# Optimization experiments

Measured on AMD Instinct MI355X. Metric: run time of the kernel, lower is better.

## Reference

```python
import jax, jax.numpy as jnp
import numpy as np
from jax import lax

# model dims (must match init_kwargs)
NB, E, G0, G1 = 1, 64, 32, 256          # num_blocks, embed_dim, grid rows, grid cols
DM, DIN, DS, DC, DTR = 2048, 4096, 16, 4, 128  # d_model, d_inner, d_state, d_conv, dt_rank
PS, ST, KD = (2, 16), (2, 16), (31, 31)
B, C, T = 8, 64, 4096


def setup_inputs() -> dict:
    key = jax.random.key(0)
    ks = jax.random.split(key, 4)
    rng = np.random.default_rng(0)

    def w(*s, fan=None):
        fan = fan if fan is not None else s[-1]
        return jnp.asarray((rng.standard_normal(s) / np.sqrt(fan)).astype(np.float32))

    # mamba_ssm-style dt bias init: softplus(bias) ~ Uniform-log in [1e-3, 0.1]
    dt = np.exp(rng.uniform(size=(NB, 2, DIN)) * (np.log(0.1) - np.log(1e-3)) + np.log(1e-3))
    dt = np.clip(dt, 1e-4, None)
    bdt = jnp.asarray((dt + np.log(-np.expm1(-dt))).astype(np.float32))
    A_log = jnp.asarray(np.broadcast_to(np.log(np.arange(1, DS + 1, dtype=np.float32)), (NB, 2, DIN, DS)).copy())

    return {
        'x': jax.random.normal(ks[0], (B, C, T), dtype=jnp.float32),
        'mask': jax.random.uniform(ks[1], (B, C, T)) < 0.5,
        'proj_w': w(E, 1, PS[0], PS[1], fan=PS[0] * PS[1]),
        'proj_b': jnp.zeros((E,), jnp.float32),
        'pos_embed': 0.02 * jax.random.normal(ks[2], (1, G1, DM), dtype=jnp.float32),
        'in_proj_w': w(NB, 2, 2 * DIN, DM, fan=DM),
        'conv_w': w(NB, 2, DIN, DC, fan=DC),
        'conv_b': jnp.zeros((NB, 2, DIN), jnp.float32),
        'x_proj_w': w(NB, 2, DTR + 2 * DS, DIN, fan=DIN),
        'dt_proj_w': w(NB, 2, DIN, DTR, fan=DTR),
        'dt_proj_b': bdt,
        'A_log': A_log,
        'Dp': jnp.ones((NB, 2, DIN), jnp.float32),
        'out_proj_w': w(NB, 2, DM, DIN, fan=DIN),
        'ln_g': jnp.ones((NB, DM), jnp.float32),
        'ln_b': jnp.zeros((NB, DM), jnp.float32),
        'dec_conv_w': w(1, 1, KD[0], KD[1], fan=KD[0] * KD[1]),
        'convT_w': w(E, 1, PS[0], PS[1], fan=E),
        'convT_b': jnp.zeros((1,), jnp.float32),
    }


def _layernorm(x, g, b, eps=1e-5):
    m = jnp.mean(x, -1, keepdims=True)
    v = jnp.var(x, -1, keepdims=True)
    return (x - m) * lax.rsqrt(v + eps) * g + b


def _mamba(h, Win, Wc, bc, Wx, Wdt, bdt, Alog, Dp, Wout):
    # h: [B, L, DM]; faithful port of mamba_ssm Mamba (selective scan reference path)
    xz = jnp.einsum('bld,ed->ble', h, Win)               # [B, L, 2*DIN]
    xc, z = jnp.split(xz, 2, axis=-1)
    xc = xc.swapaxes(1, 2)                               # [B, DIN, L]
    xc = lax.conv_general_dilated(xc, Wc[:, None, :], (1,), ((DC - 1, 0),),
                                  dimension_numbers=('NCH', 'OIH', 'NCH'),
                                  feature_group_count=DIN) + bc[None, :, None]
    u = jax.nn.silu(xc).swapaxes(1, 2)                   # [B, L, DIN]
    x_dbl = jnp.einsum('bld,ed->ble', u, Wx)             # [B, L, DTR+2*DS]
    dt = jax.nn.softplus(jnp.einsum('blr,dr->bld', x_dbl[..., :DTR], Wdt) + bdt)
    Bm = x_dbl[..., DTR:DTR + DS]                        # [B, L, DS]
    Cm = x_dbl[..., DTR + DS:]                           # [B, L, DS]
    A = -jnp.exp(Alog)                                   # [DIN, DS]

    def step(hst, inp):
        dt_t, B_t, C_t, u_t = inp                        # [B,DIN],[B,DS],[B,DS],[B,DIN]
        dA = jnp.exp(dt_t[..., None] * A)                # [B, DIN, DS]
        hst = hst * dA + (dt_t * u_t)[..., None] * B_t[:, None, :]
        return hst, jnp.einsum('bds,bs->bd', hst, C_t)

    h0 = jnp.zeros((h.shape[0], DIN, DS), h.dtype)
    xs = (dt.swapaxes(0, 1), Bm.swapaxes(0, 1), Cm.swapaxes(0, 1), u.swapaxes(0, 1))
    _, ys = lax.scan(step, h0, xs)
    y = ys.swapaxes(0, 1) + u * Dp                       # [B, L, DIN]
    y = y * jax.nn.silu(z)
    return jnp.einsum('bld,ed->ble', y, Wout)            # [B, L, DM]


def _forward(x, mask, proj_w, proj_b, pos_embed, in_proj_w, conv_w, conv_b,
             x_proj_w, dt_proj_w, dt_proj_b, A_log, Dp, out_proj_w,
             ln_g, ln_b, dec_conv_w, convT_w, convT_b):
    xm = jnp.where(mask, 0.0, x)                         # x_masked[mask] = 0
    p = lax.conv_general_dilated(xm[:, None], proj_w, ST, 'VALID',
                                 dimension_numbers=('NCHW', 'OIHW', 'NCHW'))
    p = p + proj_b[None, :, None, None]                  # [B, E, G0, G1]
    h = p.reshape(p.shape[0], E * G0, G1).transpose(0, 2, 1) + pos_embed  # [B, G1, DM]
    for i in range(NB):
        a_f = (in_proj_w[i, 0], conv_w[i, 0], conv_b[i, 0], x_proj_w[i, 0], dt_proj_w[i, 0],
               dt_proj_b[i, 0], A_log[i, 0], Dp[i, 0], out_proj_w[i, 0])
        a_r = (in_proj_w[i, 1], conv_w[i, 1], conv_b[i, 1], x_proj_w[i, 1], dt_proj_w[i, 1],
               dt_proj_b[i, 1], A_log[i, 1], Dp[i, 1], out_proj_w[i, 1])
        o = _mamba(h, *a_f) + jnp.flip(_mamba(jnp.flip(h, 1), *a_r), 1)  # bidirectional add
        h = _layernorm(h + o, ln_g[i], ln_b[i])
    # Decoder
    d = lax.conv_general_dilated(h[:, None], dec_conv_w, (1, 1),
                                 (((KD[0] - 1) // 2,) * 2, ((KD[1] - 1) // 2,) * 2),
                                 dimension_numbers=('NCHW', 'OIHW', 'NCHW'))
    d = d[:, 0].transpose(0, 2, 1).reshape(-1, E, G0, G1)
    # ConvTranspose2d(E->1, k=PS, stride=ST) as lhs-dilated conv with flipped kernel
    wct = jnp.flip(convT_w, (2, 3)).swapaxes(0, 1)       # [1, E, kh, kw]
    rec = lax.conv_general_dilated(d, wct, (1, 1),
                                   ((PS[0] - 1, PS[0] - 1), (PS[1] - 1, PS[1] - 1)),
                                   lhs_dilation=ST,
                                   dimension_numbers=('NCHW', 'OIHW', 'NCHW'))
    rec = rec + convT_b[None, :, None, None]
    return rec[:, 0], x                                  # (x_reconstructed, x_original)


def reference(x, mask, proj_w, proj_b, pos_embed, in_proj_w, conv_w, conv_b,
              x_proj_w, dt_proj_w, dt_proj_b, A_log, Dp, out_proj_w,
              ln_g, ln_b, dec_conv_w, convT_w, convT_b):
    return _forward(x, mask, proj_w, proj_b, pos_embed, in_proj_w, conv_w, conv_b,
                    x_proj_w, dt_proj_w, dt_proj_b, A_log, Dp, out_proj_w,
                    ln_g, ln_b, dec_conv_w, convT_w, convT_b)
```

## Files before the change

kernel.cpp:

```cpp
#include <hip/hip_runtime.h>
#include <hip/hip_bf16.h>
#include <math.h>

typedef unsigned short u16;
typedef __attribute__((ext_vector_type(8))) short bf16x8;
typedef __attribute__((ext_vector_type(4))) float f32x4;

__device__ __forceinline__ float b2f(u16 v) {
  unsigned u = ((unsigned)v) << 16;
  return __builtin_bit_cast(float, u);
}
__device__ __forceinline__ u16 f2b(float f) {
  unsigned u = __builtin_bit_cast(unsigned, f);
  unsigned r = u + 0x7fffu + ((u >> 16) & 1u);
  return (u16)(r >> 16);
}
__device__ __forceinline__ void gload_lds16(const u16* g, u16* l) {
  __builtin_amdgcn_global_load_lds(
      (const __attribute__((address_space(1))) void*)g,
      (__attribute__((address_space(3))) void*)l, 16, 0, 0);
}

__global__ __launch_bounds__(256) void cvt_bf16_k(const float* __restrict__ s,
                                                  u16* __restrict__ d, int n4) {
  int i = blockIdx.x * 256 + threadIdx.x;
  if (i < n4) {
    float4 v = ((const float4*)s)[i];
    ushort4 o;
    o.x = f2b(v.x); o.y = f2b(v.y); o.z = f2b(v.z); o.w = f2b(v.w);
    ((ushort4*)d)[i] = o;
  }
}

__global__ __launch_bounds__(256) void toeplitz_k(
    const float* __restrict__ kw, u16* __restrict__ tb)
{
  int i = blockIdx.x * 256 + threadIdx.x;
  if (i >= 31744) return;
  int k = i & 31, n = (i >> 5) & 15, h = (i >> 9) & 1, ki = i >> 10;
  int t = h * 32 + k - n;
  float v = (t >= 0 && t <= 30) ? kw[ki * 31 + t] : 0.f;
  tb[i] = f2b(v);
}

__global__ __launch_bounds__(256) void patchify_k(
    const float* __restrict__ x, const int* __restrict__ mask,
    const float* __restrict__ pw, const float* __restrict__ pb,
    const float* __restrict__ pos, float* __restrict__ h, u16* __restrict__ hb)
{
  int g1 = blockIdx.x, b = blockIdx.y, tid = threadIdx.x;
  __shared__ float sX[64 * 17];
  __shared__ float sW[2048];
  for (int i = tid; i < 64 * 16; i += 256) {
    int r = i >> 4, c = i & 15;
    int gi = (b * 64 + r) * 4096 + g1 * 16 + c;
    sX[r * 17 + c] = mask[gi] ? 0.f : x[gi];
  }
  for (int i = tid; i < 2048; i += 256) sW[i] = pw[i];
  __syncthreads();
  for (int m = tid; m < 2048; m += 256) {
    int e = m >> 5, g0 = m & 31;
    float acc = pb[e];
    const float* w = &sW[e * 32];
#pragma unroll
    for (int kh = 0; kh < 2; ++kh)
#pragma unroll
      for (int kw = 0; kw < 16; ++kw)
        acc += sX[(2 * g0 + kh) * 17 + kw] * w[kh * 16 + kw];
    float v = acc + pos[g1 * 2048 + m];
    long o = ((long)b * 256 + g1) * 2048 + m;
    h[o] = v;
    hb[o] = f2b(v);
  }
}

__global__ __launch_bounds__(512, 2) void gemm256_k(
    const u16* __restrict__ A0,
    const u16* __restrict__ B0, long bStride,
    u16* __restrict__ C0, long cStride,
    const float* __restrict__ cw,
    const float* __restrict__ cb,
    u16* __restrict__ ub)
{
  constexpr int K = 2048, N = 8192, LDA = 2048;
  __shared__ __align__(16) u16 lds[67584];
  u16* As = lds;
  u16* Bs = lds + 32768;
  const int dir = blockIdx.z;
  const u16* A = A0;
  const u16* B = B0 + (long)dir * bStride;
  u16* C = C0 + (long)dir * cStride;
  const int flip = dir;

  const int tid = threadIdx.x;
  const int wave = tid >> 6, lane = tid & 63;
  const int wr = wave >> 2, wc = wave & 3;
  const int bm = blockIdx.y * 256, bn = blockIdx.x * 256;
  const int lr = lane & 15, lq = lane >> 4;

  f32x4 acc[8][4];
#pragma unroll
  for (int i = 0; i < 8; ++i)
#pragma unroll
    for (int j = 0; j < 4; ++j) acc[i][j] = (f32x4){0.f, 0.f, 0.f, 0.f};

  auto stage = [&](int buf, int kt) {
    int k0 = kt << 6;
#pragma unroll
    for (int hf = 0; hf < 2; ++hf)
#pragma unroll
      for (int j = 0; j < 2; ++j) {
        int g = j * 512 + tid;
        int rl = hf * 128 + (g >> 3);
        int gr = (g & 7) ^ ((g >> 3) & 7);
        int ar = flip ? (bm + 255 - rl) : (bm + rl);
        gload_lds16(A + (long)ar * LDA + k0 + gr * 8,
                    &As[buf * 16384 + hf * 8192 + g * 8]);
        gload_lds16(B + (long)(bn + rl) * K + k0 + gr * 8,
                    &Bs[buf * 16384 + hf * 8192 + g * 8]);
      }
  };

  const int nk = K >> 6;
  stage(0, 0);
  for (int kt = 0; kt < nk; ++kt) {
    __builtin_amdgcn_s_barrier();
    __builtin_amdgcn_sched_barrier(0);
    if (kt + 1 < nk) {
      stage((kt + 1) & 1, kt + 1);
      asm volatile("s_waitcnt vmcnt(16)" ::: "memory");
    } else {
      asm volatile("s_waitcnt vmcnt(0)" ::: "memory");
    }
    __builtin_amdgcn_sched_barrier(0);
    __builtin_amdgcn_s_barrier();
    __builtin_amdgcn_sched_barrier(0);
    const int buf = kt & 1;
#pragma unroll
    for (int h = 0; h < 2; ++h) {
      bf16x8 av[8], bv[4];
#pragma unroll
      for (int i = 0; i < 8; ++i) {
        int row = wr * 128 + i * 16 + lr;
        av[i] = *(const bf16x8*)
            &As[buf * 16384 + ((row * 64 + h * 32 + lq * 8) ^ ((row & 7) << 3))];
      }
#pragma unroll
      for (int j = 0; j < 4; ++j) {
        int row = wc * 64 + j * 16 + lr;
        bv[j] = *(const bf16x8*)
            &Bs[buf * 16384 + ((row * 64 + h * 32 + lq * 8) ^ ((row & 7) << 3))];
      }
      __builtin_amdgcn_s_setprio(1);
#pragma unroll
      for (int i = 0; i < 8; ++i)
#pragma unroll
        for (int j = 0; j < 4; ++j)
          acc[i][j] = __builtin_amdgcn_mfma_f32_16x16x32_bf16(
              av[i], bv[j], acc[i][j], 0, 0, 0);
      __builtin_amdgcn_s_setprio(0);
    }
  }

  if (bn < 4096) {
    __syncthreads();
    u16* tile = lds;
#pragma unroll
    for (int i = 0; i < 8; ++i) {
      int r0 = wr * 128 + i * 16 + lq * 4;
#pragma unroll
      for (int j = 0; j < 4; ++j) {
        int col = wc * 64 + j * 16 + lr;
        f32x4 v = acc[i][j];
#pragma unroll
        for (int r = 0; r < 4; ++r)
          tile[(r0 + r) * 264 + col] = f2b(v[r]);
      }
    }
    __syncthreads();
    const int rgrp = tid >> 5, c8 = tid & 31;
    const int d0 = bn + c8 * 8;
    float wv0[8], wv1[8], wv2[8], wv3[8], cbv[8];
#pragma unroll
    for (int e = 0; e < 8; ++e) {
      const float4 wq = *(const float4*)(cw + ((long)dir * 4096 + d0 + e) * 4);
      wv0[e] = wq.x; wv1[e] = wq.y; wv2[e] = wq.z; wv3[e] = wq.w;
      cbv[e] = cb[dir * 4096 + d0 + e];
    }
    const int l0 = rgrp * 16;
    float w0[8], w1[8], w2[8];
#pragma unroll
    for (int e = 0; e < 8; ++e) { w0[e] = 0.f; w1[e] = 0.f; w2[e] = 0.f; }
    if (rgrp > 0) {
      bf16x8 t0 = *(const bf16x8*)&tile[(l0 - 3) * 264 + c8 * 8];
      bf16x8 t1 = *(const bf16x8*)&tile[(l0 - 2) * 264 + c8 * 8];
      bf16x8 t2 = *(const bf16x8*)&tile[(l0 - 1) * 264 + c8 * 8];
#pragma unroll
      for (int e = 0; e < 8; ++e) {
        w0[e] = b2f((u16)t0[e]); w1[e] = b2f((u16)t1[e]); w2[e] = b2f((u16)t2[e]);
      }
    }
    long ubase = ((long)(dir * 8 + blockIdx.y) * 256 + l0) * 4096 + d0;
#pragma unroll
    for (int l = 0; l < 16; ++l) {
      bf16x8 t = *(const bf16x8*)&tile[(l0 + l) * 264 + c8 * 8];
      float cur[8];
#pragma unroll
      for (int e = 0; e < 8; ++e) cur[e] = b2f((u16)t[e]);
      bf16x8 ov;
#pragma unroll
      for (int e = 0; e < 8; ++e) {
        float a = cbv[e] + wv0[e] * w0[e] + wv1[e] * w1[e] + wv2[e] * w2[e] +
                  wv3[e] * cur[e];
        ov[e] = (short)f2b(a / (1.f + __expf(-a)));
      }
      *(bf16x8*)(ub + ubase + (long)l * 4096) = ov;
#pragma unroll
      for (int e = 0; e < 8; ++e) { w0[e] = w1[e]; w1[e] = w2[e]; w2[e] = cur[e]; }
    }
  } else {
#pragma unroll
    for (int i = 0; i < 8; ++i) {
      int r0 = bm + wr * 128 + i * 16 + lq * 4;
#pragma unroll
      for (int j = 0; j < 4; ++j) {
        int col = bn + wc * 64 + j * 16 + lr;
        f32x4 v = acc[i][j];
#pragma unroll
        for (int r = 0; r < 4; ++r)
          C[(long)(r0 + r) * N + col] = f2b(v[r]);
      }
    }
  }
}

__global__ __launch_bounds__(512, 2) void gemm256o_k(
    const u16* __restrict__ Y0,
    const u16* __restrict__ W0,
    u16* __restrict__ part)
{
  constexpr int LDK = 4096;
  __shared__ __align__(16) u16 lds[65536];
  u16* As = lds;
  u16* Bs = lds + 32768;
  const int dir = blockIdx.z >> 1, split = blockIdx.z & 1;
  const u16* A = Y0 + (long)dir * 2048 * 4096;
  const u16* B = W0 + (long)dir * 2048 * 4096;
  u16* C = part + (long)blockIdx.z * 4194304;
  const int kbase = split << 11;

  const int tid = threadIdx.x;
  const int wave = tid >> 6, lane = tid & 63;
  const int wr = wave >> 2, wc = wave & 3;
  const int bm = blockIdx.y * 256, bn = blockIdx.x * 256;
  const int lr = lane & 15, lq = lane >> 4;

  f32x4 acc[8][4];
#pragma unroll
  for (int i = 0; i < 8; ++i)
#pragma unroll
    for (int j = 0; j < 4; ++j) acc[i][j] = (f32x4){0.f, 0.f, 0.f, 0.f};

  auto stage = [&](int buf, int kt) {
    int k0 = kbase + (kt << 6);
#pragma unroll
    for (int hf = 0; hf < 2; ++hf)
#pragma unroll
      for (int j = 0; j < 2; ++j) {
        int g = j * 512 + tid;
        int rl = hf * 128 + (g >> 3);
        int gr = (g & 7) ^ ((g >> 3) & 7);
        gload_lds16(A + (long)(bm + rl) * LDK + k0 + gr * 8,
                    &As[buf * 16384 + hf * 8192 + g * 8]);
        gload_lds16(B + (long)(bn + rl) * LDK + k0 + gr * 8,
                    &Bs[buf * 16384 + hf * 8192 + g * 8]);
      }
  };

  const int nk = 32;
  stage(0, 0);
  for (int kt = 0; kt < nk; ++kt) {
    __builtin_amdgcn_s_barrier();
    __builtin_amdgcn_sched_barrier(0);
    if (kt + 1 < nk) {
      stage((kt + 1) & 1, kt + 1);
      asm volatile("s_waitcnt vmcnt(16)" ::: "memory");
    } else {
      asm volatile("s_waitcnt vmcnt(0)" ::: "memory");
    }
    __builtin_amdgcn_sched_barrier(0);
    __builtin_amdgcn_s_barrier();
    __builtin_amdgcn_sched_barrier(0);
    const int buf = kt & 1;
#pragma unroll
    for (int h = 0; h < 2; ++h) {
      bf16x8 av[8], bv[4];
#pragma unroll
      for (int i = 0; i < 8; ++i) {
        int row = wr * 128 + i * 16 + lr;
        av[i] = *(const bf16x8*)
            &As[buf * 16384 + ((row * 64 + h * 32 + lq * 8) ^ ((row & 7) << 3))];
      }
#pragma unroll
      for (int j = 0; j < 4; ++j) {
        int row = wc * 64 + j * 16 + lr;
        bv[j] = *(const bf16x8*)
            &Bs[buf * 16384 + ((row * 64 + h * 32 + lq * 8) ^ ((row & 7) << 3))];
      }
      __builtin_amdgcn_s_setprio(1);
#pragma unroll
      for (int i = 0; i < 8; ++i)
#pragma unroll
        for (int j = 0; j < 4; ++j)
          acc[i][j] = __builtin_amdgcn_mfma_f32_16x16x32_bf16(
              av[i], bv[j], acc[i][j], 0, 0, 0);
      __builtin_amdgcn_s_setprio(0);
    }
  }

#pragma unroll
  for (int i = 0; i < 8; ++i) {
    int r0 = bm + wr * 128 + i * 16 + lq * 4;
#pragma unroll
    for (int j = 0; j < 4; ++j) {
      int col = bn + wc * 64 + j * 16 + lr;
      f32x4 v = acc[i][j];
#pragma unroll
      for (int r = 0; r < 4; ++r)
        C[(long)(r0 + r) * 2048 + col] = f2b(v[r]);
    }
  }
}

template <int EPI, int F32OUT, int BFOUT>
__global__ __launch_bounds__(256) void mfma_gemm_k(
    const u16* __restrict__ A0, long aStride,
    const u16* __restrict__ B0, long bStride,
    float* __restrict__ C0, long cStride,
    u16* __restrict__ Cb0, long cbStride,
    const float* __restrict__ bias0, int biasStride,
    int N, int K, int lda, int flipDir1)
{
  __shared__ __align__(16) u16 As[2][4096];
  __shared__ __align__(16) u16 Bs[2][4096];
  const int dir = blockIdx.z;
  const u16* A = A0 + (long)dir * aStride;
  const u16* B = B0 + (long)dir * bStride;
  float* C = F32OUT ? (C0 + (long)dir * cStride) : nullptr;
  u16* Cb = BFOUT ? (Cb0 + (long)dir * cbStride) : nullptr;
  const float* bias = (EPI == 1) ? (bias0 + (long)dir * biasStride) : nullptr;
  const int flip = flipDir1 && (dir == 1);

  const int tid = threadIdx.x;
  const int wave = tid >> 6, lane = tid & 63;
  const int wr = wave >> 1, wc = wave & 1;
  const int bm = blockIdx.y * 128, bn = blockIdx.x * 128;
  const int lr = lane & 15, lq = lane >> 4;

  f32x4 acc[4][4];
#pragma unroll
  for (int i = 0; i < 4; ++i)
#pragma unroll
    for (int j = 0; j < 4; ++j) acc[i][j] = (f32x4){0.f, 0.f, 0.f, 0.f};

  const int nk = K >> 5;

  auto stage = [&](int buf, int k0) {
#pragma unroll
    for (int iss = 0; iss < 2; ++iss) {
      int ob = wave * 2048 + iss * 1024 + lane * 16;
      int row = ob >> 6, kb = (ob >> 4) & 3;
      int rg = bm + row;
      rg = flip ? ((rg & ~255) | (255 - (rg & 255))) : rg;
      gload_lds16(A + (long)rg * lda + k0 + kb * 8,
                  &As[buf][wave * 1024 + iss * 512]);
      int rb = bn + row; rb = (rb < N) ? rb : (N - 1);
      gload_lds16(B + (long)rb * K + k0 + kb * 8,
                  &Bs[buf][wave * 1024 + iss * 512]);
    }
  };

  stage(0, 0);
  for (int kt = 0; kt < nk; ++kt) {
    __syncthreads();
    if (kt + 1 < nk) stage((kt + 1) & 1, (kt + 1) << 5);
    const int buf = kt & 1;
    bf16x8 av[4], bv[4];
#pragma unroll
    for (int i = 0; i < 4; ++i)
      av[i] = *(const bf16x8*)&As[buf][(wr * 64 + i * 16 + lr) * 32 + lq * 8];
#pragma unroll
    for (int j = 0; j < 4; ++j)
      bv[j] = *(const bf16x8*)&Bs[buf][(wc * 64 + j * 16 + lr) * 32 + lq * 8];
#pragma unroll
    for (int i = 0; i < 4; ++i)
#pragma unroll
      for (int j = 0; j < 4; ++j)
        acc[i][j] = __builtin_amdgcn_mfma_f32_16x16x32_bf16(av[i], bv[j],
                                                            acc[i][j], 0, 0, 0);
  }

#pragma unroll
  for (int i = 0; i < 4; ++i) {
    int r0 = bm + wr * 64 + i * 16 + lq * 4;
#pragma unroll
    for (int j = 0; j < 4; ++j) {
      int col = bn + wc * 64 + j * 16 + lr;
      if (col < N) {
        f32x4 v = acc[i][j];
#pragma unroll
        for (int r = 0; r < 4; ++r) {
          float xv = v[r];
          if (EPI == 1) {
            xv += bias[col];
            xv = (xv > 20.f) ? xv : log1pf(expf(xv));
          }
          if (F32OUT) C[(long)(r0 + r) * N + col] = xv;
          if (BFOUT) Cb[(long)(r0 + r) * N + col] = f2b(xv);
        }
      }
    }
  }
}

__global__ __launch_bounds__(256) void xdbl_part_k(
    const u16* __restrict__ ubf, const u16* __restrict__ Wxbf,
    float* __restrict__ part)
{
  __shared__ __align__(16) u16 As[2][4096];
  __shared__ __align__(16) u16 Bs[2][4096];
  const int dir = blockIdx.z >> 2, split = blockIdx.z & 3;
  const u16* A = ubf + (long)dir * 2048 * 4096;
  const u16* B = Wxbf + (long)dir * 160 * 4096;
  float* C = part + (long)blockIdx.z * 327680;
  const int tid = threadIdx.x;
  const int wave = tid >> 6, lane = tid & 63;
  const int wr = wave >> 1, wc = wave & 1;
  const int bm = blockIdx.y * 128, bn = blockIdx.x * 128;
  const int lr = lane & 15, lq = lane >> 4;

  f32x4 acc[4][4];
#pragma unroll
  for (int i = 0; i < 4; ++i)
#pragma unroll
    for (int j = 0; j < 4; ++j) acc[i][j] = (f32x4){0.f, 0.f, 0.f, 0.f};

  auto stage = [&](int buf, int k0) {
#pragma unroll
    for (int iss = 0; iss < 2; ++iss) {
      int ob = wave * 2048 + iss * 1024 + lane * 16;
      int row = ob >> 6, kb = (ob >> 4) & 3;
      gload_lds16(A + (long)(bm + row) * 4096 + k0 + kb * 8,
                  &As[buf][wave * 1024 + iss * 512]);
      int rb = bn + row; rb = (rb < 160) ? rb : 159;
      gload_lds16(B + (long)rb * 4096 + k0 + kb * 8,
                  &Bs[buf][wave * 1024 + iss * 512]);
    }
  };

  const int kbase = split << 10;
  stage(0, kbase);
  for (int kt = 0; kt < 32; ++kt) {
    __syncthreads();
    if (kt + 1 < 32) stage((kt + 1) & 1, kbase + ((kt + 1) << 5));
    const int buf = kt & 1;
    bf16x8 av[4], bv[4];
#pragma unroll
    for (int i = 0; i < 4; ++i)
      av[i] = *(const bf16x8*)&As[buf][(wr * 64 + i * 16 + lr) * 32 + lq * 8];
#pragma unroll
    for (int j = 0; j < 4; ++j)
      bv[j] = *(const bf16x8*)&Bs[buf][(wc * 64 + j * 16 + lr) * 32 + lq * 8];
#pragma unroll
    for (int i = 0; i < 4; ++i)
#pragma unroll
      for (int j = 0; j < 4; ++j)
        acc[i][j] = __builtin_amdgcn_mfma_f32_16x16x32_bf16(av[i], bv[j],
                                                            acc[i][j], 0, 0, 0);
  }

#pragma unroll
  for (int i = 0; i < 4; ++i) {
    int r0 = bm + wr * 64 + i * 16 + lq * 4;
#pragma unroll
    for (int j = 0; j < 4; ++j) {
      int col = bn + wc * 64 + j * 16 + lr;
      if (col < 160) {
        f32x4 v = acc[i][j];
#pragma unroll
        for (int r = 0; r < 4; ++r)
          C[(long)(r0 + r) * 160 + col] = v[r];
      }
    }
  }
}

__global__ __launch_bounds__(256) void xdbl_reduce_k(
    const float* __restrict__ part, float* __restrict__ xdbl,
    u16* __restrict__ xdbl_bf)
{
  int i = blockIdx.x * 256 + threadIdx.x;
  if (i >= 655360) return;
  int dir = i / 327680, rem = i - dir * 327680;
  long pb = (long)dir * 4 * 327680 + rem;
  float s = part[pb] + part[pb + 327680] + part[pb + 2 * 327680] +
            part[pb + 3 * 327680];
  xdbl[i] = s;
  xdbl_bf[i] = f2b(s);
}

__global__ __launch_bounds__(256) void scan_a_k(
    const u16* __restrict__ dtbuf, const u16* __restrict__ ubuf,
    const float* __restrict__ xdbl, const float* __restrict__ A_log,
    const float* __restrict__ Dpv, u16* __restrict__ ypre,
    float* __restrict__ stend, float* __restrict__ dtsum)
{
  int blk = blockIdx.x;
  int dtile = blk & 15, c = (blk >> 4) & 7, b = (blk >> 7) & 7, dir = blk >> 10;
  int tid = threadIdx.x;
  int d = dtile * 256 + tid;
  int db = dir * 8 + b;

  __shared__ float sB[32][16], sC[32][16];
  long r160 = (long)db * 256 * 160;
  for (int i = tid; i < 1024; i += 256) {
    int l = i >> 5, s = i & 31;
    float v = xdbl[r160 + (long)(c * 32 + l) * 160 + 128 + s];
    if (s < 16) sB[l][s] = v; else sC[l][s - 16] = v;
  }
  __syncthreads();

  float A[16], st[16];
  const float4* ap = (const float4*)(A_log + ((long)dir * 4096 + d) * 16);
#pragma unroll
  for (int q = 0; q < 4; ++q) {
    float4 t = ap[q];
    A[q * 4 + 0] = -__expf(t.x); A[q * 4 + 1] = -__expf(t.y);
    A[q * 4 + 2] = -__expf(t.z); A[q * 4 + 3] = -__expf(t.w);
  }
#pragma unroll
  for (int s = 0; s < 16; ++s) st[s] = 0.f;
  float Dpd = Dpv[dir * 4096 + d];

  long base = (long)db * 256 * 4096 + (long)c * 32 * 4096 + d;
  float dts = 0.f;
  for (int i = 0; i < 32; ++i) {
    float dtv = b2f(dtbuf[base + (long)i * 4096]);
    float uv  = b2f(ubuf[base + (long)i * 4096]);
    dts += dtv;
    float du = dtv * uv;
    float y = 0.f;
#pragma unroll
    for (int s = 0; s < 16; ++s) {
      st[s] = st[s] * __expf(dtv * A[s]) + du * sB[i][s];
      y += st[s] * sC[i][s];
    }
    ypre[base + (long)i * 4096] = f2b(y + uv * Dpd);
  }
  long eb = ((long)(db * 8 + c) * 4096 + d) * 16;
  float4* ep = (float4*)(stend + eb);
#pragma unroll
  for (int q = 0; q < 4; ++q)
    ep[q] = make_float4(st[q * 4], st[q * 4 + 1], st[q * 4 + 2], st[q * 4 + 3]);
  dtsum[(long)(db * 8 + c) * 4096 + d] = dts;
}

__global__ __launch_bounds__(512) void scan_b_k(
    const u16* __restrict__ dtbuf, const u16* __restrict__ xzbf,
    const float* __restrict__ xdbl, const float* __restrict__ A_log,
    const float* __restrict__ stend, const float* __restrict__ dtsum,
    u16* __restrict__ ybuf)
{
  int blk = blockIdx.x;
  int dtile = blk & 63, b = (blk >> 6) & 7, dir = blk >> 9;
  int tid = threadIdx.x;
  int c = tid >> 6, dd = tid & 63;
  int d0 = dtile * 64, d = d0 + dd;
  int db = dir * 8 + b;

  __shared__ float sEnd[8][64][17];
  __shared__ float sT[8][64];
  __shared__ float sC[256][16];

  long eBase = (long)db * 8 * 65536;
  for (int i = tid; i < 8192; i += 512) {
    int cc = i >> 10, rem = i & 1023, dd2 = rem >> 4, s = rem & 15;
    sEnd[cc][dd2][s] = stend[eBase + (long)cc * 65536 + (long)(d0 + dd2) * 16 + s];
  }
  {
    int cc = tid >> 6, dd2 = tid & 63;
    sT[cc][dd2] = dtsum[(long)(db * 8 + cc) * 4096 + d0 + dd2];
  }
  long r160 = (long)db * 256 * 160;
  for (int i = tid; i < 4096; i += 512) {
    int l = i >> 4, s = i & 15;
    sC[l][s] = xdbl[r160 + (long)l * 160 + 144 + s];
  }
  __syncthreads();

  float A[16];
  const float4* ap = (const float4*)(A_log + ((long)dir * 4096 + d) * 16);
#pragma unroll
  for (int q = 0; q < 4; ++q) {
    float4 t = ap[q];
    A[q * 4 + 0] = -__expf(t.x); A[q * 4 + 1] = -__expf(t.y);
    A[q * 4 + 2] = -__expf(t.z); A[q * 4 + 3] = -__expf(t.w);
  }
  float g[16];
#pragma unroll
  for (int s = 0; s < 16; ++s) g[s] = 0.f;
  for (int j = 0; j < c; ++j) {
    float Tj = sT[j][dd];
#pragma unroll
    for (int s = 0; s < 16; ++s)
      g[s] = g[s] * __expf(A[s] * Tj) + sEnd[j][dd][s];
  }

  long base  = (long)db * 256 * 4096 + (long)c * 32 * 4096 + d;
  long zbase = (long)db * 256 * 8192 + (long)c * 32 * 8192 + 4096 + d;
  float cum = 0.f;
  if (c == 0) {
    for (int i = 0; i < 32; ++i) {
      float yp = b2f(ybuf[base + (long)i * 4096]);
      float zv = b2f(xzbf[zbase + (long)i * 8192]);
      float y = yp * (zv / (1.f + __expf(-zv)));
      ybuf[base + (long)i * 4096] = f2b(y);
    }
  } else {
    for (int i = 0; i < 32; ++i) {
      float dtv = b2f(dtbuf[base + (long)i * 4096]);
      cum += dtv;
      float yp = b2f(ybuf[base + (long)i * 4096]);
      float corr = 0.f;
      const int l = c * 32 + i;
#pragma unroll
      for (int s = 0; s < 16; ++s)
        corr += sC[l][s] * __expf(A[s] * cum) * g[s];
      float zv = b2f(xzbf[zbase + (long)i * 8192]);
      float y = (yp + corr) * (zv / (1.f + __expf(-zv)));
      ybuf[base + (long)i * 4096] = f2b(y);
    }
  }
}

__global__ __launch_bounds__(256) void add_ln_k(
    const float* __restrict__ h, const u16* __restrict__ op,
    const float* __restrict__ g, const float* __restrict__ bta,
    u16* __restrict__ h2b)
{
  int row = blockIdx.x;
  int b = row >> 8, l = row & 255;
  long base = (long)row * 2048;
  long base1 = ((long)b * 256 + (255 - l)) * 2048;
  int t8 = threadIdx.x * 8;
  const u16* p0 = op;
  const u16* p1 = op + 4194304;
  const u16* p2 = op + 2L * 4194304;
  const u16* p3 = op + 3L * 4194304;
  float v[8];
  float4 x0 = *(const float4*)(h + base + t8);
  float4 x1 = *(const float4*)(h + base + t8 + 4);
  bf16x8 a8 = *(const bf16x8*)(p0 + base + t8);
  bf16x8 b8 = *(const bf16x8*)(p1 + base + t8);
  bf16x8 c8v = *(const bf16x8*)(p2 + base1 + t8);
  bf16x8 d8 = *(const bf16x8*)(p3 + base1 + t8);
  const float* xp = (const float*)&x0;
  float xv[8] = {x0.x, x0.y, x0.z, x0.w, x1.x, x1.y, x1.z, x1.w};
  (void)xp;
#pragma unroll
  for (int j = 0; j < 8; ++j)
    v[j] = xv[j] + b2f((u16)a8[j]) + b2f((u16)b8[j]) + b2f((u16)c8v[j]) +
           b2f((u16)d8[j]);
  float s = 0.f, ss = 0.f;
#pragma unroll
  for (int j = 0; j < 8; ++j) { s += v[j]; ss += v[j] * v[j]; }
#pragma unroll
  for (int off = 32; off >= 1; off >>= 1) {
    s += __shfl_xor(s, off, 64);
    ss += __shfl_xor(ss, off, 64);
  }
  __shared__ float red[8];
  int wid = threadIdx.x >> 6, lane = threadIdx.x & 63;
  if (lane == 0) { red[wid] = s; red[wid + 4] = ss; }
  __syncthreads();
  if (threadIdx.x == 0) {
    red[0] = red[0] + red[1] + red[2] + red[3];
    red[4] = red[4] + red[5] + red[6] + red[7];
  }
  __syncthreads();
  float mean = red[0] * (1.f / 2048.f);
  float var = red[4] * (1.f / 2048.f) - mean * mean;
  float inv = rsqrtf(var + 1e-5f);
  bf16x8 o;
#pragma unroll
  for (int j = 0; j < 8; ++j)
    o[j] = (short)f2b((v[j] - mean) * inv * g[t8 + j] + bta[t8 + j]);
  *(bf16x8*)(h2b + base + t8) = o;
}

__global__ __launch_bounds__(256) void dec_conv31_k(
    const u16* __restrict__ h2b, const u16* __restrict__ tb,
    float* __restrict__ dc)
{
  __shared__ __align__(16) u16 sIn[94 * 120];
  const int b = blockIdx.z;
  const int l0 = blockIdx.y * 64;
  const int m0 = blockIdx.x * 64;
  const int tid = threadIdx.x;
  const u16* src = h2b + (long)b * 256 * 2048;
  for (int i = tid; i < 94 * 112; i += 256) {
    int r = i / 112, c = i - r * 112;
    int gl = l0 + r - 15, gm = m0 + c - 15;
    u16 v = 0;
    if (gl >= 0 && gl < 256 && gm >= 0 && gm < 2048)
      v = src[(long)gl * 2048 + gm];
    sIn[r * 120 + c] = v;
  }
  __syncthreads();
  const int wave = tid >> 6, lane = tid & 63;
  const int lr = lane & 15, lq = lane >> 4;

  f32x4 acc[4];
#pragma unroll
  for (int s = 0; s < 4; ++s) acc[s] = (f32x4){0.f, 0.f, 0.f, 0.f};

#pragma unroll 1
  for (int ki = 0; ki < 31; ++ki) {
    const u16* arow = &sIn[(wave * 16 + lr + ki) * 120];
#pragma unroll
    for (int h = 0; h < 2; ++h) {
      bf16x8 bv = *(const bf16x8*)&tb[((ki * 2 + h) * 16 + lr) * 32 + lq * 8];
#pragma unroll
      for (int ms = 0; ms < 4; ++ms) {
        bf16x8 av = *(const bf16x8*)&arow[ms * 16 + h * 32 + lq * 8];
        acc[ms] = __builtin_amdgcn_mfma_f32_16x16x32_bf16(av, bv, acc[ms], 0, 0, 0);
      }
    }
  }
#pragma unroll
  for (int ms = 0; ms < 4; ++ms) {
    f32x4 v = acc[ms];
#pragma unroll
    for (int r = 0; r < 4; ++r)
      dc[((long)b * 256 + l0 + wave * 16 + lq * 4 + r) * 2048 + m0 + ms * 16 + lr]
          = v[r];
  }
}

__global__ __launch_bounds__(256) void convT_k(
    const float* __restrict__ dc, const float* __restrict__ w,
    const float* __restrict__ wb, float* __restrict__ out)
{
  int j = blockIdx.x, b = blockIdx.y;
  __shared__ float sD[2048];
  __shared__ float sW[2048];
  int tid = threadIdx.x;
  const float* drow = dc + ((long)b * 256 + j) * 2048;
  for (int i = tid; i < 2048; i += 256) { sD[i] = drow[i]; sW[i] = w[i]; }
  __syncthreads();
  float cb = wb[0];
  int owlo = tid & 15, ohbase = tid >> 4;
#pragma unroll
  for (int q = 0; q < 4; ++q) {
    int oh = ohbase + q * 16;
    int i = oh >> 1, a = oh & 1;
    float acc = cb;
#pragma unroll 8
    for (int e = 0; e < 64; ++e)
      acc += sD[e * 32 + i] * sW[e * 32 + a * 16 + owlo];
    out[((long)b * 64 + oh) * 4096 + j * 16 + owlo] = acc;
  }
}

extern "C" void kernel_launch(void* const* d_in, const int* in_sizes, int n_in,
                              void* d_out, int out_size, void* d_ws, size_t ws_size,
                              hipStream_t stream)
{
  const float* x      = (const float*)d_in[0];
  const int*   mask   = (const int*)d_in[1];
  const float* proj_w = (const float*)d_in[2];
  const float* proj_b = (const float*)d_in[3];
  const float* pos    = (const float*)d_in[4];
  const float* Wip    = (const float*)d_in[5];
  const float* convw  = (const float*)d_in[6];
  const float* convb  = (const float*)d_in[7];
  const float* Wx     = (const float*)d_in[8];
  const float* Wdt    = (const float*)d_in[9];
  const float* bdt    = (const float*)d_in[10];
  const float* Alog   = (const float*)d_in[11];
  const float* Dpv    = (const float*)d_in[12];
  const float* Wout   = (const float*)d_in[13];
  const float* lng    = (const float*)d_in[14];
  const float* lnb    = (const float*)d_in[15];
  const float* dkw    = (const float*)d_in[16];
  const float* ctw    = (const float*)d_in[17];
  const float* ctb    = (const float*)d_in[18];
  float* out = (float*)d_out;

  char* p = (char*)d_ws;
  u16*   xz_bf   = (u16*)p;
  p += 67108864;
  u16*   u_bf    = (u16*)p;
  float* dc      = (float*)p;
  p += 33554432;
  u16*   dt_bf   = (u16*)p; p += 67108864;
  float* xdbl    = (float*)p; p += 2621440;
  u16*   xdbl_bf = (u16*)p;  p += 1310720;
  float* h       = (float*)p; p += 16777216;
  u16*   h_bf    = (u16*)p;  p += 8388608;
  float* h2      = (float*)p; p += 16777216;
  u16*   y_bf    = (u16*)p;  p += 33554432;
  u16*   Wpool   = (u16*)p;  p += 67108864;
  u16*   Wx_bf   = (u16*)p;  p += 2621440;
  u16*   Wdt_bf  = (u16*)p;  p += 2097152;
  u16*   tb      = (u16*)p;  p += 65536;
  u16*   h2b     = (u16*)p;  p += 8388608;

  float* part    = (float*)(Wpool + 16777216);
  float* st_end  = (float*)(Wpool + 16777216);
  float* dtsum   = h2;
  u16*   opart   = dt_bf;

  cvt_bf16_k<<<32768, 256, 0, stream>>>(Wip, Wpool, 8388608);
  cvt_bf16_k<<<1280, 256, 0, stream>>>(Wx, Wx_bf, 327680);
  cvt_bf16_k<<<1024, 256, 0, stream>>>(Wdt, Wdt_bf, 262144);
  toeplitz_k<<<124, 256, 0, stream>>>(dkw, tb);

  patchify_k<<<dim3(256, 8), 256, 0, stream>>>(x, mask, proj_w, proj_b, pos, h, h_bf);

  gemm256_k<<<dim3(32, 8, 2), 512, 0, stream>>>(
      h_bf, Wpool, (long)8192 * 2048, xz_bf, (long)2048 * 8192,
      convw, convb, u_bf);

  xdbl_part_k<<<dim3(2, 16, 8), 256, 0, stream>>>(u_bf, Wx_bf, part);
  xdbl_reduce_k<<<2560, 256, 0, stream>>>(part, xdbl, xdbl_bf);

  mfma_gemm_k<1, 0, 1><<<dim3(32, 16, 2), 256, 0, stream>>>(
      xdbl_bf, (long)2048 * 160, Wdt_bf, (long)4096 * 128, nullptr, 0L,
      dt_bf, (long)2048 * 4096, bdt, 4096, 4096, 128, 160, 0);

  scan_a_k<<<2048, 256, 0, stream>>>(dt_bf, u_bf, xdbl, Alog, Dpv, y_bf, st_end, dtsum);
  scan_b_k<<<1024, 512, 0, stream>>>(dt_bf, xz_bf, xdbl, Alog, st_end, dtsum, y_bf);

  cvt_bf16_k<<<16384, 256, 0, stream>>>(Wout, Wpool, 4194304);

  gemm256o_k<<<dim3(8, 8, 4), 512, 0, stream>>>(y_bf, Wpool, opart);

  add_ln_k<<<2048, 256, 0, stream>>>(h, opart, lng, lnb, h2b);

  dec_conv31_k<<<dim3(32, 4, 8), 256, 0, stream>>>(h2b, tb, dc);

  convT_k<<<dim3(256, 8), 256, 0, stream>>>(dc, ctw, ctb, out);

  hipMemcpyAsync(out + 2097152, x, (size_t)2097152 * 4,
                 hipMemcpyDeviceToDevice, stream);
}
```

Baseline: 593.5 us.

## Merge prep kernels, drop fp32 residual, bf16 dec-conv output, swizzle GEMM blocks

Merges three small conversion and Toeplitz kernels into one launch. Stops writing the fp32 residual h and reads the bf16 copy in add_ln instead. Stores the decoder conv output as bf16, which halves its write and read traffic. Remaps block indices in both big GEMMs so that adjacent workgroups spread across tiles, aiming at better L2/MALL locality. The bf16 residual and bf16 dec-conv intermediate lower precision and may push the error closer to tolerance.

Result: faster. 580.7 us (-2.2%).

```diff
diff --git a/kernel.cpp b/kernel.cpp
--- a/kernel.cpp
+++ b/kernel.cpp
@@ -32,21 +32,38 @@
   }
 }
 
-__global__ __launch_bounds__(256) void toeplitz_k(
+__global__ __launch_bounds__(256) void prep_k(
+    const float* __restrict__ Wx, u16* __restrict__ Wxb,
+    const float* __restrict__ Wdt, u16* __restrict__ Wdtb,
     const float* __restrict__ kw, u16* __restrict__ tb)
 {
   int i = blockIdx.x * 256 + threadIdx.x;
-  if (i >= 31744) return;
-  int k = i & 31, n = (i >> 5) & 15, h = (i >> 9) & 1, ki = i >> 10;
-  int t = h * 32 + k - n;
-  float v = (t >= 0 && t <= 30) ? kw[ki * 31 + t] : 0.f;
-  tb[i] = f2b(v);
+  if (i < 327680) {
+    float4 v = ((const float4*)Wx)[i];
+    ushort4 o;
+    o.x = f2b(v.x); o.y = f2b(v.y); o.z = f2b(v.z); o.w = f2b(v.w);
+    ((ushort4*)Wxb)[i] = o;
+  } else if (i < 589824) {
+    int j = i - 327680;
+    float4 v = ((const float4*)Wdt)[j];
+    ushort4 o;
+    o.x = f2b(v.x); o.y = f2b(v.y); o.z = f2b(v.z); o.w = f2b(v.w);
+    ((ushort4*)Wdtb)[j] = o;
+  } else {
+    int j = i - 589824;
+    if (j < 31744) {
+      int k = j & 31, n = (j >> 5) & 15, hh = (j >> 9) & 1, ki = j >> 10;
+      int t = hh * 32 + k - n;
+      float v = (t >= 0 && t <= 30) ? kw[ki * 31 + t] : 0.f;
+      tb[j] = f2b(v);
+    }
+  }
 }
 
 __global__ __launch_bounds__(256) void patchify_k(
     const float* __restrict__ x, const int* __restrict__ mask,
     const float* __restrict__ pw, const float* __restrict__ pb,
-    const float* __restrict__ pos, float* __restrict__ h, u16* __restrict__ hb)
+    const float* __restrict__ pos, u16* __restrict__ hb)
 {
   int g1 = blockIdx.x, b = blockIdx.y, tid = threadIdx.x;
   __shared__ float sX[64 * 17];
@@ -68,9 +85,7 @@
       for (int kw = 0; kw < 16; ++kw)
         acc += sX[(2 * g0 + kh) * 17 + kw] * w[kh * 16 + kw];
     float v = acc + pos[g1 * 2048 + m];
-    long o = ((long)b * 256 + g1) * 2048 + m;
-    h[o] = v;
-    hb[o] = f2b(v);
+    hb[((long)b * 256 + g1) * 2048 + m] = f2b(v);
   }
 }
 
@@ -86,7 +101,9 @@
   __shared__ __align__(16) u16 lds[67584];
   u16* As = lds;
   u16* Bs = lds + 32768;
-  const int dir = blockIdx.z;
+  const int lin = (int)(blockIdx.z * 256 + blockIdx.y * 32 + blockIdx.x);
+  const int swz = (lin & 7) * 64 + (lin >> 3);
+  const int nbx = swz & 31, nby = (swz >> 5) & 7, dir = swz >> 8;
   const u16* A = A0;
   const u16* B = B0 + (long)dir * bStride;
   u16* C = C0 + (long)dir * cStride;
@@ -95,7 +112,7 @@
   const int tid = threadIdx.x;
   const int wave = tid >> 6, lane = tid & 63;
   const int wr = wave >> 2, wc = wave & 3;
-  const int bm = blockIdx.y * 256, bn = blockIdx.x * 256;
+  const int bm = nby * 256, bn = nbx * 256;
   const int lr = lane & 15, lq = lane >> 4;
 
   f32x4 acc[8][4];
@@ -200,7 +217,7 @@
         w0[e] = b2f((u16)t0[e]); w1[e] = b2f((u16)t1[e]); w2[e] = b2f((u16)t2[e]);
       }
     }
-    long ubase = ((long)(dir * 8 + blockIdx.y) * 256 + l0) * 4096 + d0;
+    long ubase = ((long)(dir * 8 + nby) * 256 + l0) * 4096 + d0;
 #pragma unroll
     for (int l = 0; l < 16; ++l) {
       bf16x8 t = *(const bf16x8*)&tile[(l0 + l) * 264 + c8 * 8];
@@ -243,16 +260,19 @@
   __shared__ __align__(16) u16 lds[65536];
   u16* As = lds;
   u16* Bs = lds + 32768;
-  const int dir = blockIdx.z >> 1, split = blockIdx.z & 1;
+  const int lin = (int)(blockIdx.z * 64 + blockIdx.y * 8 + blockIdx.x);
+  const int swz = (lin & 7) * 32 + (lin >> 3);
+  const int nbx = swz & 7, nby = (swz >> 3) & 7, nz = swz >> 6;
+  const int dir = nz >> 1, split = nz & 1;
   const u16* A = Y0 + (long)dir * 2048 * 4096;
   const u16* B = W0 + (long)dir * 2048 * 4096;
-  u16* C = part + (long)blockIdx.z * 4194304;
+  u16* C = part + (long)nz * 4194304;
   const int kbase = split << 11;
 
   const int tid = threadIdx.x;
   const int wave = tid >> 6, lane = tid & 63;
   const int wr = wave >> 2, wc = wave & 3;
-  const int bm = blockIdx.y * 256, bn = blockIdx.x * 256;
+  const int bm = nby * 256, bn = nbx * 256;
   const int lr = lane & 15, lq = lane >> 4;
 
   f32x4 acc[8][4];
@@ -644,7 +664,7 @@
 }
 
 __global__ __launch_bounds__(256) void add_ln_k(
-    const float* __restrict__ h, const u16* __restrict__ op,
+    const u16* __restrict__ hb, const u16* __restrict__ op,
     const float* __restrict__ g, const float* __restrict__ bta,
     u16* __restrict__ h2b)
 {
@@ -658,19 +678,15 @@
   const u16* p2 = op + 2L * 4194304;
   const u16* p3 = op + 3L * 4194304;
   float v[8];
-  float4 x0 = *(const float4*)(h + base + t8);
-  float4 x1 = *(const float4*)(h + base + t8 + 4);
+  bf16x8 x8 = *(const bf16x8*)(hb + base + t8);
   bf16x8 a8 = *(const bf16x8*)(p0 + base + t8);
   bf16x8 b8 = *(const bf16x8*)(p1 + base + t8);
   bf16x8 c8v = *(const bf16x8*)(p2 + base1 + t8);
   bf16x8 d8 = *(const bf16x8*)(p3 + base1 + t8);
-  const float* xp = (const float*)&x0;
-  float xv[8] = {x0.x, x0.y, x0.z, x0.w, x1.x, x1.y, x1.z, x1.w};
-  (void)xp;
 #pragma unroll
   for (int j = 0; j < 8; ++j)
-    v[j] = xv[j] + b2f((u16)a8[j]) + b2f((u16)b8[j]) + b2f((u16)c8v[j]) +
-           b2f((u16)d8[j]);
+    v[j] = b2f((u16)x8[j]) + b2f((u16)a8[j]) + b2f((u16)b8[j]) +
+           b2f((u16)c8v[j]) + b2f((u16)d8[j]);
   float s = 0.f, ss = 0.f;
 #pragma unroll
   for (int j = 0; j < 8; ++j) { s += v[j]; ss += v[j] * v[j]; }
@@ -700,7 +716,7 @@
 
 __global__ __launch_bounds__(256) void dec_conv31_k(
     const u16* __restrict__ h2b, const u16* __restrict__ tb,
-    float* __restrict__ dc)
+    u16* __restrict__ dc)
 {
   __shared__ __align__(16) u16 sIn[94 * 120];
   const int b = blockIdx.z;
@@ -743,20 +759,20 @@
 #pragma unroll
     for (int r = 0; r < 4; ++r)
       dc[((long)b * 256 + l0 + wave * 16 + lq * 4 + r) * 2048 + m0 + ms * 16 + lr]
-          = v[r];
+          = f2b(v[r]);
   }
 }
 
 __global__ __launch_bounds__(256) void convT_k(
-    const float* __restrict__ dc, const float* __restrict__ w,
+    const u16* __restrict__ dc, const float* __restrict__ w,
     const float* __restrict__ wb, float* __restrict__ out)
 {
   int j = blockIdx.x, b = blockIdx.y;
   __shared__ float sD[2048];
   __shared__ float sW[2048];
   int tid = threadIdx.x;
-  const float* drow = dc + ((long)b * 256 + j) * 2048;
-  for (int i = tid; i < 2048; i += 256) { sD[i] = drow[i]; sW[i] = w[i]; }
+  const u16* drow = dc + ((long)b * 256 + j) * 2048;
+  for (int i = tid; i < 2048; i += 256) { sD[i] = b2f(drow[i]); sW[i] = w[i]; }
   __syncthreads();
   float cb = wb[0];
   int owlo = tid & 15, ohbase = tid >> 4;
@@ -801,12 +817,11 @@
   u16*   xz_bf   = (u16*)p;
   p += 67108864;
   u16*   u_bf    = (u16*)p;
-  float* dc      = (float*)p;
+  u16*   dc      = (u16*)p;
   p += 33554432;
   u16*   dt_bf   = (u16*)p; p += 67108864;
   float* xdbl    = (float*)p; p += 2621440;
   u16*   xdbl_bf = (u16*)p;  p += 1310720;
-  float* h       = (float*)p; p += 16777216;
   u16*   h_bf    = (u16*)p;  p += 8388608;
   float* h2      = (float*)p; p += 16777216;
   u16*   y_bf    = (u16*)p;  p += 33554432;
@@ -822,11 +837,9 @@
   u16*   opart   = dt_bf;
 
   cvt_bf16_k<<<32768, 256, 0, stream>>>(Wip, Wpool, 8388608);
-  cvt_bf16_k<<<1280, 256, 0, stream>>>(Wx, Wx_bf, 327680);
-  cvt_bf16_k<<<1024, 256, 0, stream>>>(Wdt, Wdt_bf, 262144);
-  toeplitz_k<<<124, 256, 0, stream>>>(dkw, tb);
-
-  patchify_k<<<dim3(256, 8), 256, 0, stream>>>(x, mask, proj_w, proj_b, pos, h, h_bf);
+  prep_k<<<2428, 256, 0, stream>>>(Wx, Wx_bf, Wdt, Wdt_bf, dkw, tb);
+
+  patchify_k<<<dim3(256, 8), 256, 0, stream>>>(x, mask, proj_w, proj_b, pos, h_bf);
 
   gemm256_k<<<dim3(32, 8, 2), 512, 0, stream>>>(
       h_bf, Wpool, (long)8192 * 2048, xz_bf, (long)2048 * 8192,
@@ -846,7 +859,7 @@
 
   gemm256o_k<<<dim3(8, 8, 4), 512, 0, stream>>>(y_bf, Wpool, opart);
 
-  add_ln_k<<<2048, 256, 0, stream>>>(h, opart, lng, lnb, h2b);
+  add_ln_k<<<2048, 256, 0, stream>>>(h_bf, opart, lng, lnb, h2b);
 
   dec_conv31_k<<<dim3(32, 4, 8), 256, 0, stream>>>(h2b, tb, dc);
 
```
